# Performance work log

Measured on AMD Instinct MI355X. Metric: run time of the kernel, lower is better.

The kernel has to match this reference:

```python
import jax, jax.numpy as jnp
import numpy as np

B, N, C = 2, 2048, 768
H, HD = 12, 64
HID = 3072
LN_EPS = 1e-5
POL_EPS = 1e-6


def _layer_norm(x, g, b):
    m = jnp.mean(x, axis=-1, keepdims=True)
    v = jnp.mean(jnp.square(x - m), axis=-1, keepdims=True)
    return (x - m) * jax.lax.rsqrt(v + LN_EPS) * g + b


def _softmax_with_policy(attn, policy):
    # attn: [B,H,N,N], policy: [B,N,1]
    n = attn.shape[-1]
    ap = policy.reshape(policy.shape[0], 1, 1, n)  # [B,1,1,N]
    eye = jnp.eye(n, dtype=ap.dtype)[None, None]   # [1,1,N,N]
    ap = ap + (1.0 - ap) * eye                     # always attend to self
    attn = attn - jnp.max(attn, axis=-1, keepdims=True)
    attn = jnp.exp(attn.astype(jnp.float32)) * ap.astype(jnp.float32)
    attn = (attn + POL_EPS / n) / (jnp.sum(attn, axis=-1, keepdims=True) + POL_EPS)
    return attn


def setup_inputs() -> dict:
    key = jax.random.key(0)
    ks = jax.random.split(key, 12)
    s = lambda fan_in: 1.0 / np.sqrt(fan_in)
    x = jax.random.normal(ks[0], (B, N, C), dtype=jnp.float32)
    policy = (jax.random.uniform(ks[1], (B, N, 1)) > 0.5).astype(jnp.float32)
    return {
        "x": x,
        "policy": policy,
        "ln1_g": jnp.ones((C,), jnp.float32),
        "ln1_b": jnp.zeros((C,), jnp.float32),
        "qkv_w": jax.random.uniform(ks[2], (3 * H * HD, C), jnp.float32, -s(C), s(C)),
        "proj_w": jax.random.uniform(ks[3], (C, H * HD), jnp.float32, -s(H * HD), s(H * HD)),
        "proj_b": jnp.zeros((C,), jnp.float32),
        "ln2_g": jnp.ones((C,), jnp.float32),
        "ln2_b": jnp.zeros((C,), jnp.float32),
        "fc1_w": jax.random.uniform(ks[4], (HID, C), jnp.float32, -s(C), s(C)),
        "fc1_b": jnp.zeros((HID,), jnp.float32),
        "fc2_w": jax.random.uniform(ks[5], (C, HID), jnp.float32, -s(HID), s(HID)),
        "fc2_b": jnp.zeros((C,), jnp.float32),
    }


def reference(x, policy, ln1_g, ln1_b, qkv_w, proj_w, proj_b, ln2_g, ln2_b, fc1_w, fc1_b, fc2_w, fc2_b):
    b, n, c = x.shape
    scale = HD ** -0.5
    # --- attention branch (pre-LN) ---
    h = _layer_norm(x, ln1_g, ln1_b)
    qkv = (h @ qkv_w.T).reshape(b, n, 3, H, HD).transpose(2, 0, 3, 1, 4)  # [3,B,H,N,hd]
    q, k, v = qkv[0], qkv[1], qkv[2]
    attn = jnp.einsum("bhqd,bhkd->bhqk", q * scale, k)
    attn = _softmax_with_policy(attn, policy).astype(x.dtype)
    o = jnp.einsum("bhqk,bhkd->bhqd", attn, v).transpose(0, 2, 1, 3).reshape(b, n, H * HD)
    x = x + (o @ proj_w.T + proj_b)  # skip_lam = 1.0, dropout/drop_path = identity
    # --- MLP branch (pre-LN) ---
    h = _layer_norm(x, ln2_g, ln2_b)
    h = jax.nn.gelu(h @ fc1_w.T + fc1_b, approximate=False)  # torch nn.GELU = exact erf
    x = x + (h @ fc2_w.T + fc2_b)
    return x
```

## Files before the change

kernel.cpp:

```cpp
#include <hip/hip_runtime.h>

typedef unsigned short u16;
typedef unsigned int u32;
typedef float f32x4 __attribute__((ext_vector_type(4)));
typedef float f32x16 __attribute__((ext_vector_type(16)));
typedef __bf16 bf16x8 __attribute__((ext_vector_type(8)));
typedef u16 u16x4v __attribute__((ext_vector_type(4)));
typedef u32 u32x2 __attribute__((ext_vector_type(2)));
typedef u32 u32x4 __attribute__((ext_vector_type(4)));

#define NHEAD 12
#define NN 2048
#define CC 768

#define GLOBAL_AS __attribute__((address_space(1)))
#define LDS_AS __attribute__((address_space(3)))

__device__ __forceinline__ u16 tobf(float f) {
  __bf16 h = (__bf16)f;
  return __builtin_bit_cast(u16, h);
}
__device__ __forceinline__ float bf2f(u16 h) {
  u32 u = ((u32)h) << 16;
  return __builtin_bit_cast(float, u);
}
__device__ __forceinline__ u32 cvtpk(float lo, float hi) {
  u32 r;
  asm("v_cvt_pk_bf16_f32 %0, %1, %2" : "=v"(r) : "v"(lo), "v"(hi));
  return r;
}
__device__ __forceinline__ void plswap(u32& a, u32& b) {
  asm volatile("v_permlane32_swap_b32 %0, %1" : "+v"(a), "+v"(b));
}
__device__ __forceinline__ void plswapf(float& a, float& b) {
  asm volatile("v_permlane32_swap_b32 %0, %1" : "+v"(a), "+v"(b));
}

#define N4_QKV 442368
#define N4_PROJ 147456
#define N4_FC 589824
__global__ __launch_bounds__(256) void cvt4_kernel(
    const float* __restrict__ a, const float* __restrict__ b,
    const float* __restrict__ c, const float* __restrict__ d,
    u16* __restrict__ oa, u16* __restrict__ ob, u16* __restrict__ oc,
    u16* __restrict__ od) {
  int i = blockIdx.x * 256 + threadIdx.x;
  const float* src;
  u16* dst;
  if (i < N4_QKV) {
    src = a; dst = oa;
  } else if (i < N4_QKV + N4_PROJ) {
    i -= N4_QKV; src = b; dst = ob;
  } else if (i < N4_QKV + N4_PROJ + N4_FC) {
    i -= N4_QKV + N4_PROJ; src = c; dst = oc;
  } else {
    i -= N4_QKV + N4_PROJ + N4_FC; src = d; dst = od;
    if (i >= N4_FC) return;
  }
  float4 v = ((const float4*)src)[i];
  u16x4v o = {tobf(v.x), tobf(v.y), tobf(v.z), tobf(v.w)};
  ((u16x4v*)dst)[i] = o;
}

__global__ __launch_bounds__(256) void ln_kernel(const float* __restrict__ x,
                                                 const float* __restrict__ gw,
                                                 const float* __restrict__ bw,
                                                 u16* __restrict__ out) {
  int row = blockIdx.x * 4 + (threadIdx.x >> 6);
  int lane = threadIdx.x & 63;
  const float* xr = x + (size_t)row * CC + lane * 12;
  float v[12];
  *(float4*)&v[0] = *(const float4*)(xr + 0);
  *(float4*)&v[4] = *(const float4*)(xr + 4);
  *(float4*)&v[8] = *(const float4*)(xr + 8);
  float s = 0.f, sq = 0.f;
#pragma unroll
  for (int j = 0; j < 12; ++j) { s += v[j]; sq += v[j] * v[j]; }
#pragma unroll
  for (int o = 1; o < 64; o <<= 1) { s += __shfl_xor(s, o); sq += __shfl_xor(sq, o); }
  float mean = s * (1.f / CC);
  float var = sq * (1.f / CC) - mean * mean;
  float rs = rsqrtf(var + 1e-5f);
  u16 ob[12];
#pragma unroll
  for (int j = 0; j < 12; ++j) {
    int c = lane * 12 + j;
    ob[j] = tobf((v[j] - mean) * rs * gw[c] + bw[c]);
  }
  u32* orow = (u32*)(out + (size_t)row * CC + lane * 12);
#pragma unroll
  for (int j = 0; j < 6; ++j) orow[j] = (u32)ob[2 * j] | ((u32)ob[2 * j + 1] << 16);
}

template <int BM, int OB, int HASB, int ACT, int RES>
__global__ __launch_bounds__(256) void gemm_kernel(
    const u16* __restrict__ A, const u16* __restrict__ Bw,
    const float* __restrict__ bias, const float* __restrict__ res,
    void* __restrict__ Cout, int M, int N, int K) {
  constexpr int MW = BM / 2;
  constexpr int MF = MW / 16;
  __shared__ __align__(16) u16 Alds[BM * 64];
  __shared__ __align__(16) u16 Blds[128 * 64];
  const int tid = threadIdx.x;
  const int lane = tid & 63, wave = tid >> 6;
  const int l15 = lane & 15, g = lane >> 4;
  const int nx = gridDim.x;
  const int flat = blockIdx.y * nx + blockIdx.x;
  const int cpx = (nx * gridDim.y) >> 3;
  const int swz = (flat & 7) * cpx + (flat >> 3);
  const int bm = (swz % nx) * BM, bn = (swz / nx) * 128;
  const int wm = (wave >> 1) * MW, wn = (wave & 1) * 64;
  f32x4 acc[MF][4] = {};

  for (int kt = 0; kt < K; kt += 64) {
#pragma unroll
    for (int i = 0; i < BM / 32; ++i) {
      int ob_ = i * 4096 + wave * 1024;
      int lb = ob_ + lane * 16;
      int row = lb >> 7;
      int cb = (lb & 127) ^ ((row & 7) << 4);
      const u16* sa = A + (size_t)(bm + row) * K + kt + (cb >> 1);
      __builtin_amdgcn_global_load_lds((const GLOBAL_AS void*)sa,
                                       (LDS_AS void*)(Alds + (ob_ >> 1)), 16, 0, 0);
    }
#pragma unroll
    for (int i = 0; i < 4; ++i) {
      int ob_ = i * 4096 + wave * 1024;
      int lb = ob_ + lane * 16;
      int row = lb >> 7;
      int cb = (lb & 127) ^ ((row & 7) << 4);
      const u16* sb = Bw + (size_t)(bn + row) * K + kt + (cb >> 1);
      __builtin_amdgcn_global_load_lds((const GLOBAL_AS void*)sb,
                                       (LDS_AS void*)(Blds + (ob_ >> 1)), 16, 0, 0);
    }
    __syncthreads();
#pragma unroll
    for (int ks = 0; ks < 2; ++ks) {
      bf16x8 af[MF], bfr[4];
#pragma unroll
      for (int mi = 0; mi < MF; ++mi) {
        int row = wm + mi * 16 + l15;
        int cb = (ks * 64 + g * 16) ^ ((row & 7) << 4);
        af[mi] = *(const bf16x8*)&Alds[row * 64 + (cb >> 1)];
      }
#pragma unroll
      for (int ni = 0; ni < 4; ++ni) {
        int row = wn + ni * 16 + l15;
        int cb = (ks * 64 + g * 16) ^ ((row & 7) << 4);
        bfr[ni] = *(const bf16x8*)&Blds[row * 64 + (cb >> 1)];
      }
#pragma unroll
      for (int mi = 0; mi < MF; ++mi)
#pragma unroll
        for (int ni = 0; ni < 4; ++ni)
          acc[mi][ni] = __builtin_amdgcn_mfma_f32_16x16x32_bf16(af[mi], bfr[ni],
                                                                acc[mi][ni], 0, 0, 0);
    }
    __syncthreads();
  }
#pragma unroll
  for (int mi = 0; mi < MF; ++mi) {
#pragma unroll
    for (int ni = 0; ni < 4; ++ni) {
      int col = bn + wn + ni * 16 + l15;
      float bs = HASB ? bias[col] : 0.f;
#pragma unroll
      for (int r = 0; r < 4; ++r) {
        int rowm = bm + wm + mi * 16 + g * 4 + r;
        float v = acc[mi][ni][r] + bs;
        if (ACT) v = 0.5f * v * (1.f + erff(v * 0.70710678118654752f));
        if (RES) v += res[(size_t)rowm * N + col];
        if (OB)
          ((u16*)Cout)[(size_t)rowm * N + col] = tobf(v);
        else
          ((float*)Cout)[(size_t)rowm * N + col] = v;
      }
    }
  }
}

__global__ __launch_bounds__(256) void vsum_kernel(const u16* __restrict__ qkv,
                                                   float* __restrict__ vs) {
  int bh = blockIdx.x, q4 = blockIdx.y;
  int b = bh / NHEAD, h = bh % NHEAD;
  int d = threadIdx.x & 63, part = threadIdx.x >> 6;
  float s = 0.f;
  for (int n = q4 * 512 + part; n < q4 * 512 + 512; n += 4)
    s += bf2f(qkv[(size_t)(b * NN + n) * 2304 + 2 * CC + h * 64 + d]);
  __shared__ float red[256];
  red[threadIdx.x] = s;
  __syncthreads();
  if (threadIdx.x < 64) {
    float t = red[threadIdx.x] + red[threadIdx.x + 64] + red[threadIdx.x + 128] +
              red[threadIdx.x + 192];
    vs[q4 * (24 * 64) + bh * 64 + threadIdx.x] = t;
  }
}

__global__ __launch_bounds__(256) void scan_kernel(const float* __restrict__ policy,
                                                   int* __restrict__ ncbuf,
                                                   int* __restrict__ idxbuf) {
  int b = blockIdx.x, tid = threadIdx.x;
  float pv[8];
  *(float4*)&pv[0] = *(const float4*)&policy[b * NN + tid * 8];
  *(float4*)&pv[4] = *(const float4*)&policy[b * NN + tid * 8 + 4];
  int cnt = 0;
#pragma unroll
  for (int j = 0; j < 8; ++j) cnt += (pv[j] != 0.f) ? 1 : 0;
  __shared__ int sc[256];
  sc[tid] = cnt;
  __syncthreads();
  for (int off = 1; off < 256; off <<= 1) {
    int v = sc[tid];
    int add = (tid >= off) ? sc[tid - off] : 0;
    __syncthreads();
    sc[tid] = v + add;
    __syncthreads();
  }
  int base = sc[tid] - cnt;
#pragma unroll
  for (int j = 0; j < 8; ++j) {
    if (pv[j] != 0.f) idxbuf[b * NN + base++] = tid * 8 + j;
  }
  if (tid == 255) ncbuf[b] = sc[255];
}

__global__ __launch_bounds__(256) void gather_kernel(const u16* __restrict__ qkv,
                                                     const int* __restrict__ ncbuf,
                                                     const int* __restrict__ idxbuf,
                                                     u16* __restrict__ ckv) {
  int b = blockIdx.y;
  int nc = ncbuf[b];
  int ncp = (nc + 127) & ~127;
  int c = blockIdx.x * 256 + threadIdx.x;
  int j = c / 192, col = (c % 192) * 8;
  if (j >= ncp) return;
  uint4 val = {0, 0, 0, 0};
  if (j < nc) {
    int src = idxbuf[b * NN + j];
    val = *(const uint4*)&qkv[(size_t)(b * NN + src) * 2304 + CC + col];
  }
  *(uint4*)&ckv[(size_t)(b * NN + j) * 1536 + col] = val;
}

#define SCL2E 0.18033688f
#define TRRD(dst, addr, OFF) \
  asm volatile("ds_read_b64_tr_b16 %0, %1 offset:" OFF : "=v"(dst) : "v"(addr))

__global__ __launch_bounds__(256) void attn32_kernel(const u16* __restrict__ qkv,
                                                     const u16* __restrict__ ckv,
                                                     const int* __restrict__ ncbuf,
                                                     float* __restrict__ partO,
                                                     float* __restrict__ partlm) {
  __shared__ __align__(16) u16 Klds[2][4096];
  __shared__ __align__(16) u16 Vlds[2][4096];
  __shared__ float alf[4][32];
  const int bh = blockIdx.y, b = bh / NHEAD, h = bh % NHEAD;
  const int qt = blockIdx.x >> 1, half = blockIdx.x & 1;
  const int tid = threadIdx.x, lane = tid & 63, w = tid >> 6;
  const int l31 = lane & 31, hp = lane >> 5, b4 = (lane >> 4) & 1;
  const int q0 = qt * 128 + w * 32;
  const int nc = ncbuf[b];
  const int ncp = (nc + 127) & ~127;
  const int nh = ncp >> 1;
  const int nt = nh >> 6;
  const int kv0 = half * nh;
  const size_t adv = (size_t)64 * 1536;

  bf16x8 qf0, qf1, qf2, qf3;
  {
    const u16* qp = qkv + (size_t)(b * NN + q0 + l31) * 2304 + h * 64 + 8 * hp;
#pragma unroll
    for (int ds = 0; ds < 4; ++ds) {
      bf16x8 r = *(const bf16x8*)(qp + ds * 16);
      bf16x8 o;
#pragma unroll
      for (int j = 0; j < 8; ++j) o[j] = (__bf16)((float)r[j] * SCL2E);
      if (ds == 0) qf0 = o; else if (ds == 1) qf1 = o; else if (ds == 2) qf2 = o; else qf3 = o;
    }
  }

  const u16* ksrc[2];
  const u16* vsrcp[2];
#pragma unroll
  for (int c = 0; c < 2; ++c) {
    int lb = c * 4096 + w * 1024 + lane * 16;
    int row = lb >> 7;
    int cb = (lb & 127) ^ ((row & 7) << 4);
    ksrc[c] = ckv + (size_t)(b * NN + kv0 + row) * 1536 + h * 64 + (cb >> 1);
    int idx0 = (c * 256 + w * 64 + lane) * 8;
    int s0 = idx0 & 15, jj = (idx0 >> 4) & 3, b4v = (idx0 >> 6) & 1,
        pv = (idx0 >> 7) & 1, hv = (idx0 >> 8) & 1, dtv = (idx0 >> 9) & 1,
        mkv = (idx0 >> 10) & 3;
    int key = mkv * 16 + 8 * hv + 4 * pv + jj;
    int d0 = dtv * 32 + 16 * b4v + s0;
    vsrcp[c] = ckv + (size_t)(b * NN + kv0 + key) * 1536 + CC + h * 64 + d0;
  }
  auto stage = [&](int buf) {
#pragma unroll
    for (int c = 0; c < 2; ++c) {
      __builtin_amdgcn_global_load_lds((const GLOBAL_AS void*)ksrc[c],
                                       (LDS_AS void*)&Klds[buf][c * 2048 + w * 512], 16, 0, 0);
      __builtin_amdgcn_global_load_lds((const GLOBAL_AS void*)vsrcp[c],
                                       (LDS_AS void*)&Vlds[buf][c * 2048 + w * 512], 16, 0, 0);
      ksrc[c] += adv; vsrcp[c] += adv;
    }
  };

  stage(0);
  __syncthreads();

  float m_cur = -3.0e38f, m_true = -3.0e38f, l_run = 0.f;
  f32x16 accd[2] = {};
  const u32 vbase = (u32)(uintptr_t)(LDS_AS u16*)&Vlds[0][0] +
                    (u32)(2 * (lane & 15) + 128 * b4 + 512 * hp);

#pragma unroll 1
  for (int t = 0; t < nt; ++t) {
    const int cur = t & 1;
    if (t < nt - 1) stage(cur ^ 1);

    f32x16 sv0, sv1;
    {
      bf16x8 kf[4];
#pragma unroll
      for (int ds = 0; ds < 4; ++ds) {
        int row = l31;
        int cb = (32 * ds + 16 * hp) ^ ((row & 7) << 4);
        kf[ds] = *(const bf16x8*)((const char*)&Klds[cur][0] + row * 128 + cb);
      }
      f32x16 a = {};
      a = __builtin_amdgcn_mfma_f32_32x32x16_bf16(kf[0], qf0, a, 0, 0, 0);
      a = __builtin_amdgcn_mfma_f32_32x32x16_bf16(kf[1], qf1, a, 0, 0, 0);
      a = __builtin_amdgcn_mfma_f32_32x32x16_bf16(kf[2], qf2, a, 0, 0, 0);
      a = __builtin_amdgcn_mfma_f32_32x32x16_bf16(kf[3], qf3, a, 0, 0, 0);
      sv0 = a;
    }
    {
      bf16x8 kf[4];
#pragma unroll
      for (int ds = 0; ds < 4; ++ds) {
        int row = 32 + l31;
        int cb = (32 * ds + 16 * hp) ^ ((row & 7) << 4);
        kf[ds] = *(const bf16x8*)((const char*)&Klds[cur][0] + row * 128 + cb);
      }
      f32x16 a = {};
      a = __builtin_amdgcn_mfma_f32_32x32x16_bf16(kf[0], qf0, a, 0, 0, 0);
      a = __builtin_amdgcn_mfma_f32_32x32x16_bf16(kf[1], qf1, a, 0, 0, 0);
      a = __builtin_amdgcn_mfma_f32_32x32x16_bf16(kf[2], qf2, a, 0, 0, 0);
      a = __builtin_amdgcn_mfma_f32_32x32x16_bf16(kf[3], qf3, a, 0, 0, 0);
      sv1 = a;
    }

    u32x2 tr[4][2][2];
    {
      u32 vab = vbase + (u32)(cur * 8192);
      TRRD(tr[0][0][0], vab, "0");    TRRD(tr[0][0][1], vab, "256");
      TRRD(tr[0][1][0], vab, "1024"); TRRD(tr[0][1][1], vab, "1280");
      TRRD(tr[1][0][0], vab, "2048"); TRRD(tr[1][0][1], vab, "2304");
      TRRD(tr[1][1][0], vab, "3072"); TRRD(tr[1][1][1], vab, "3328");
      TRRD(tr[2][0][0], vab, "4096"); TRRD(tr[2][0][1], vab, "4352");
      TRRD(tr[3][0][0], vab, "6144"); TRRD(tr[3][0][1], vab, "6400");
      TRRD(tr[2][1][0], vab, "5120"); TRRD(tr[2][1][1], vab, "5376");
      TRRD(tr[3][1][0], vab, "7168"); TRRD(tr[3][1][1], vab, "7424");
    }

    float ta = fmaxf(fmaxf(sv0[0], sv0[1]), sv0[2]);
    float tb = fmaxf(fmaxf(sv0[3], sv0[4]), sv0[5]);
    float tc = fmaxf(fmaxf(sv0[6], sv0[7]), sv0[8]);
    float td = fmaxf(fmaxf(sv0[9], sv0[10]), sv0[11]);
    float te = fmaxf(fmaxf(sv0[12], sv0[13]), sv0[14]);
    float tf = fmaxf(fmaxf(sv0[15], sv1[0]), sv1[1]);
    float tg = fmaxf(fmaxf(sv1[2], sv1[3]), sv1[4]);
    float th = fmaxf(fmaxf(sv1[5], sv1[6]), sv1[7]);
    float ti = fmaxf(fmaxf(sv1[8], sv1[9]), sv1[10]);
    float tj = fmaxf(fmaxf(sv1[11], sv1[12]), sv1[13]);
    float tk = fmaxf(sv1[14], sv1[15]);
    float tmax = fmaxf(fmaxf(fmaxf(fmaxf(ta, tb), fmaxf(tc, td)),
                             fmaxf(fmaxf(te, tf), fmaxf(tg, th))),
                       fmaxf(fmaxf(ti, tj), tk));
    {
      float t1 = tmax, t2 = tmax;
      plswapf(t1, t2);
      tmax = fmaxf(t1, t2);
    }
    m_true = fmaxf(m_true, tmax);
    const bool defer = __all(tmax <= m_cur + 8.f);
    const float m_new = defer ? m_cur : fmaxf(m_cur, tmax);

    const int thr = nc - (kv0 + t * 64);
    float ev[32];
#pragma unroll
    for (int kt = 0; kt < 2; ++kt) {
#pragma unroll
      for (int i = 0; i < 4; ++i) {
#pragma unroll
        for (int rq = 0; rq < 4; ++rq) {
          int r = 4 * i + rq;
          int kidx = kt * 32 + 8 * i + 4 * hp + rq;
          float sval = kt ? sv1[r] : sv0[r];
          float e = __builtin_amdgcn_exp2f(sval - m_new);
          ev[kt * 16 + r] = (kidx < thr) ? e : 0.f;
        }
      }
    }
    u32 wv[16];
#pragma unroll
    for (int j = 0; j < 16; ++j) wv[j] = cvtpk(ev[2 * j], ev[2 * j + 1]);
    float ps[16];
#pragma unroll
    for (int j = 0; j < 16; ++j)
      ps[j] = __builtin_bit_cast(float, wv[j] << 16) +
              __builtin_bit_cast(float, wv[j] & 0xffff0000u);
#pragma unroll
    for (int s = 8; s > 0; s >>= 1)
#pragma unroll
      for (int j = 0; j < s; ++j) ps[j] += ps[j + s];
    float psum = ps[0];
    {
      float s1 = psum, s2 = psum;
      plswapf(s1, s2);
      psum = s1 + s2;
    }
    if (!defer) {
      float alpha = __builtin_amdgcn_exp2f(m_cur - m_new);
      l_run = l_run * alpha + psum;
      m_cur = m_new;
      if (lane < 32) alf[w][lane] = alpha;
      float4 aq0 = *(const float4*)&alf[w][4 * hp];
      float4 aq1 = *(const float4*)&alf[w][8 + 4 * hp];
      float4 aq2 = *(const float4*)&alf[w][16 + 4 * hp];
      float4 aq3 = *(const float4*)&alf[w][24 + 4 * hp];
#pragma unroll
      for (int dt = 0; dt < 2; ++dt) {
#pragma unroll
        for (int rq = 0; rq < 4; ++rq) {
          accd[dt][0 + rq] *= ((const float*)&aq0)[rq];
          accd[dt][4 + rq] *= ((const float*)&aq1)[rq];
          accd[dt][8 + rq] *= ((const float*)&aq2)[rq];
          accd[dt][12 + rq] *= ((const float*)&aq3)[rq];
        }
      }
    } else {
      l_run += psum;
    }

    u32 PK[4][4];
#pragma unroll
    for (int mk = 0; mk < 4; ++mk) {
      int bw_ = 8 * (mk >> 1) + 4 * (mk & 1);
      PK[mk][0] = wv[bw_ + 0];
      PK[mk][1] = wv[bw_ + 1];
      PK[mk][2] = wv[bw_ + 2];
      PK[mk][3] = wv[bw_ + 3];
      plswap(PK[mk][2], PK[mk][0]);
      plswap(PK[mk][3], PK[mk][1]);
    }

    asm volatile("s_waitcnt lgkmcnt(0)" ::: "memory");
    __builtin_amdgcn_sched_barrier(0);

#pragma unroll
    for (int mk = 0; mk < 4; ++mk) {
      u32x4 pk4 = {PK[mk][0], PK[mk][1], PK[mk][2], PK[mk][3]};
      bf16x8 pf = __builtin_bit_cast(bf16x8, pk4);
#pragma unroll
      for (int dt = 0; dt < 2; ++dt) {
        u32x4 vv = {tr[mk][dt][0].x, tr[mk][dt][0].y, tr[mk][dt][1].x, tr[mk][dt][1].y};
        bf16x8 vf = __builtin_bit_cast(bf16x8, vv);
        accd[dt] = __builtin_amdgcn_mfma_f32_32x32x16_bf16(pf, vf, accd[dt], 0, 0, 0);
      }
    }
    __syncthreads();
  }

  float sr = __builtin_amdgcn_exp2f(m_cur - m_true);
  if (lane < 32) {
    alf[w][lane] = sr;
    float2 lm = {l_run * sr, m_true};
    *(float2*)&partlm[2 * ((size_t)(half * 24 + bh) * 2048 + q0 + lane)] = lm;
  }
  float4 sq0 = *(const float4*)&alf[w][4 * hp];
  float4 sq1 = *(const float4*)&alf[w][8 + 4 * hp];
  float4 sq2 = *(const float4*)&alf[w][16 + 4 * hp];
  float4 sq3 = *(const float4*)&alf[w][24 + 4 * hp];
  float* pb2 = partO + ((size_t)(half * 24 + bh) * 2048) * 64;
#pragma unroll
  for (int dt = 0; dt < 2; ++dt) {
#pragma unroll
    for (int i = 0; i < 4; ++i) {
      float4 sqv = (i == 0) ? sq0 : (i == 1) ? sq1 : (i == 2) ? sq2 : sq3;
#pragma unroll
      for (int rq = 0; rq < 4; ++rq) {
        int row = q0 + 8 * i + 4 * hp + rq;
        pb2[(size_t)row * 64 + dt * 32 + l31] = accd[dt][4 * i + rq] * ((const float*)&sqv)[rq];
      }
    }
  }
}

__global__ __launch_bounds__(256) void merge_kernel(const float* __restrict__ partO,
                                                    const float* __restrict__ partlm,
                                                    const float* __restrict__ vs,
                                                    const float* __restrict__ policy,
                                                    const u16* __restrict__ qkv,
                                                    u16* __restrict__ o) {
  int rr = blockIdx.x * 4 + (threadIdx.x >> 6);
  int lane = threadIdx.x & 63;
  int bh = rr >> 11, q = rr & 2047;
  int b = bh / NHEAD, h = bh % NHEAD;
  const float* O1 = partO + ((size_t)bh * 2048 + q) * 64;
  const float* O2 = partO + ((size_t)(24 + bh) * 2048 + q) * 64;
  float2 lm1 = ((const float2*)partlm)[(size_t)bh * 2048 + q];
  float2 lm2 = ((const float2*)partlm)[(size_t)(24 + bh) * 2048 + q];
  float ms = fmaxf(lm1.y, lm2.y);
  float w1 = exp2f(lm1.y - ms), w2 = exp2f(lm2.y - ms);
  float num_d = 0.f, den_d = 0.f;
  if (policy[b * NN + q] == 0.f) {
    const u16* rowp = qkv + (size_t)(b * NN + q) * 2304 + h * 64 + lane;
    float qd = bf2f(rowp[0]);
    float kd = bf2f(rowp[CC]);
    float vv = bf2f(rowp[2 * CC]);
    float dp = qd * kd;
#pragma unroll
    for (int of = 1; of < 64; of <<= 1) dp += __shfl_xor(dp, of);
    float e = exp2f(dp * 0.18033688f - ms);
    num_d = e * vv;
    den_d = e;
  }
  float den = lm1.x * w1 + lm2.x * w2 + den_d + 1e-6f;
  float vsv = vs[bh * 64 + lane] + vs[1536 + bh * 64 + lane] +
              vs[3072 + bh * 64 + lane] + vs[4608 + bh * 64 + lane];
  float num = O1[lane] * w1 + O2[lane] * w2 + num_d + (1e-6f / 2048.f) * vsv;
  o[((size_t)(b * NN + q)) * CC + h * 64 + lane] = tobf(num / den);
}

extern "C" void kernel_launch(void* const* d_in, const int* in_sizes, int n_in,
                              void* d_out, int out_size, void* d_ws, size_t ws_size,
                              hipStream_t stream) {
  const float* x = (const float*)d_in[0];
  const float* policy = (const float*)d_in[1];
  const float* ln1g = (const float*)d_in[2];
  const float* ln1b = (const float*)d_in[3];
  const float* qkvw = (const float*)d_in[4];
  const float* projw = (const float*)d_in[5];
  const float* projb = (const float*)d_in[6];
  const float* ln2g = (const float*)d_in[7];
  const float* ln2b = (const float*)d_in[8];
  const float* fc1w = (const float*)d_in[9];
  const float* fc1b = (const float*)d_in[10];
  const float* fc2w = (const float*)d_in[11];
  const float* fc2b = (const float*)d_in[12];
  float* out = (float*)d_out;

  char* ws = (char*)d_ws;
  size_t off = 0;
  auto alloc = [&](size_t bytes) {
    void* p = ws + off;
    off = (off + bytes + 255) & ~(size_t)255;
    return p;
  };
  u16* wq = (u16*)alloc((size_t)2304 * 768 * 2);
  u16* wp = (u16*)alloc((size_t)768 * 768 * 2);
  u16* w1 = (u16*)alloc((size_t)3072 * 768 * 2);
  u16* w2 = (u16*)alloc((size_t)768 * 3072 * 2);
  u16* hbuf = (u16*)alloc((size_t)4096 * 768 * 2);
  u16* obuf = (u16*)alloc((size_t)4096 * 768 * 2);
  u16* qkv = (u16*)alloc((size_t)4096 * 2304 * 2);
  float* vs = (float*)alloc((size_t)4 * 24 * 64 * 4);
  int* ncbuf = (int*)alloc(2 * sizeof(int));
  int* idxbuf = (int*)alloc((size_t)2 * NN * sizeof(int));
  size_t unionOff = off;
  float* partO = (float*)alloc((size_t)2 * 24 * 2048 * 64 * 4);
  float* partlm = (float*)alloc((size_t)2 * 24 * 2048 * 2 * 4);
  float* x1 = (float*)(ws + unionOff);
  u16* ckv = hbuf;
  u16* f1 = obuf;

  cvt4_kernel<<<6912, 256, 0, stream>>>(qkvw, projw, fc1w, fc2w, wq, wp, w1, w2);

  ln_kernel<<<1024, 256, 0, stream>>>(x, ln1g, ln1b, hbuf);
  gemm_kernel<128, 1, 0, 0, 0><<<dim3(32, 18), 256, 0, stream>>>(
      hbuf, wq, nullptr, nullptr, qkv, 4096, 2304, 768);
  vsum_kernel<<<dim3(24, 4), 256, 0, stream>>>(qkv, vs);
  scan_kernel<<<2, 256, 0, stream>>>(policy, ncbuf, idxbuf);
  gather_kernel<<<dim3(1536, 2), 256, 0, stream>>>(qkv, ncbuf, idxbuf, ckv);
  attn32_kernel<<<dim3(32, 24), 256, 0, stream>>>(qkv, ckv, ncbuf, partO, partlm);
  merge_kernel<<<12288, 256, 0, stream>>>(partO, partlm, vs, policy, qkv, obuf);
  gemm_kernel<64, 0, 1, 0, 1><<<dim3(64, 6), 256, 0, stream>>>(
      obuf, wp, projb, x, x1, 4096, 768, 768);
  ln_kernel<<<1024, 256, 0, stream>>>(x1, ln2g, ln2b, hbuf);
  gemm_kernel<128, 1, 1, 1, 0><<<dim3(32, 24), 256, 0, stream>>>(
      hbuf, w1, fc1b, nullptr, f1, 4096, 3072, 768);
  gemm_kernel<64, 0, 1, 0, 1><<<dim3(64, 6), 256, 0, stream>>>(
      f1, w2, fc2b, x1, out, 4096, 768, 3072);
}
```

Before: 232.0 us.

## Double-buffer GEMM LDS tiles with async prefetch and use polynomial erf GELU

Splits the GEMM shared-memory tiles into two buffers. The next K-tile's global-to-LDS loads are issued before computing on the current tile, with explicit vmcnt waits and raw barriers replacing __syncthreads, so load latency overlaps MFMA work. The exact erff in the fused GELU epilogue is replaced by a rational polynomial approximation using hardware rcp and exp2. This doubles LDS use per block, which may lower occupancy, and introduces a small approximation error in GELU.

```diff
diff --git a/kernel.cpp b/kernel.cpp
--- a/kernel.cpp
+++ b/kernel.cpp
@@ -34,6 +34,19 @@
 }
 __device__ __forceinline__ void plswapf(float& a, float& b) {
   asm volatile("v_permlane32_swap_b32 %0, %1" : "+v"(a), "+v"(b));
+}
+__device__ __forceinline__ float gelu_erf(float v) {
+  float y = fabsf(v) * 0.70710678118654752f;
+  float t = __builtin_amdgcn_rcpf(fmaf(0.3275911f, y, 1.f));
+  float p = fmaf(1.061405429f, t, -1.453152027f);
+  p = fmaf(p, t, 1.421413741f);
+  p = fmaf(p, t, -0.284496736f);
+  p = fmaf(p, t, 0.254829592f);
+  p = p * t;
+  float e = __builtin_amdgcn_exp2f(-y * y * 1.44269504f);
+  float er = fmaf(-p, e, 1.f);
+  er = (v < 0.f) ? -er : er;
+  return 0.5f * v * (1.f + er);
 }
 
 #define N4_QKV 442368
@@ -99,8 +112,8 @@
     void* __restrict__ Cout, int M, int N, int K) {
   constexpr int MW = BM / 2;
   constexpr int MF = MW / 16;
-  __shared__ __align__(16) u16 Alds[BM * 64];
-  __shared__ __align__(16) u16 Blds[128 * 64];
+  __shared__ __align__(16) u16 Alds[2][BM * 64];
+  __shared__ __align__(16) u16 Blds[2][128 * 64];
   const int tid = threadIdx.x;
   const int lane = tid & 63, wave = tid >> 6;
   const int l15 = lane & 15, g = lane >> 4;
@@ -112,7 +125,7 @@
   const int wm = (wave >> 1) * MW, wn = (wave & 1) * 64;
   f32x4 acc[MF][4] = {};
 
-  for (int kt = 0; kt < K; kt += 64) {
+  auto stage = [&](int buf, int kt) {
 #pragma unroll
     for (int i = 0; i < BM / 32; ++i) {
       int ob_ = i * 4096 + wave * 1024;
@@ -121,7 +134,7 @@
       int cb = (lb & 127) ^ ((row & 7) << 4);
       const u16* sa = A + (size_t)(bm + row) * K + kt + (cb >> 1);
       __builtin_amdgcn_global_load_lds((const GLOBAL_AS void*)sa,
-                                       (LDS_AS void*)(Alds + (ob_ >> 1)), 16, 0, 0);
+                                       (LDS_AS void*)(&Alds[buf][0] + (ob_ >> 1)), 16, 0, 0);
     }
 #pragma unroll
     for (int i = 0; i < 4; ++i) {
@@ -131,9 +144,28 @@
       int cb = (lb & 127) ^ ((row & 7) << 4);
       const u16* sb = Bw + (size_t)(bn + row) * K + kt + (cb >> 1);
       __builtin_amdgcn_global_load_lds((const GLOBAL_AS void*)sb,
-                                       (LDS_AS void*)(Blds + (ob_ >> 1)), 16, 0, 0);
-    }
-    __syncthreads();
+                                       (LDS_AS void*)(&Blds[buf][0] + (ob_ >> 1)), 16, 0, 0);
+    }
+  };
+
+  const int nt = K >> 6;
+  stage(0, 0);
+#pragma unroll 1
+  for (int t = 0; t < nt; ++t) {
+    const int cur = t & 1;
+    if (t + 1 < nt) {
+      stage(cur ^ 1, (t + 1) * 64);
+      if constexpr (BM == 128) {
+        asm volatile("s_waitcnt vmcnt(8)" ::: "memory");
+      } else {
+        asm volatile("s_waitcnt vmcnt(6)" ::: "memory");
+      }
+    } else {
+      asm volatile("s_waitcnt vmcnt(0)" ::: "memory");
+    }
+    __builtin_amdgcn_sched_barrier(0);
+    __builtin_amdgcn_s_barrier();
+    __builtin_amdgcn_sched_barrier(0);
 #pragma unroll
     for (int ks = 0; ks < 2; ++ks) {
       bf16x8 af[MF], bfr[4];
@@ -141,13 +173,13 @@
       for (int mi = 0; mi < MF; ++mi) {
         int row = wm + mi * 16 + l15;
         int cb = (ks * 64 + g * 16) ^ ((row & 7) << 4);
-        af[mi] = *(const bf16x8*)&Alds[row * 64 + (cb >> 1)];
+        af[mi] = *(const bf16x8*)&Alds[cur][row * 64 + (cb >> 1)];
       }
 #pragma unroll
       for (int ni = 0; ni < 4; ++ni) {
         int row = wn + ni * 16 + l15;
         int cb = (ks * 64 + g * 16) ^ ((row & 7) << 4);
-        bfr[ni] = *(const bf16x8*)&Blds[row * 64 + (cb >> 1)];
+        bfr[ni] = *(const bf16x8*)&Blds[cur][row * 64 + (cb >> 1)];
       }
 #pragma unroll
       for (int mi = 0; mi < MF; ++mi)
@@ -156,7 +188,10 @@
           acc[mi][ni] = __builtin_amdgcn_mfma_f32_16x16x32_bf16(af[mi], bfr[ni],
                                                                 acc[mi][ni], 0, 0, 0);
     }
-    __syncthreads();
+    asm volatile("s_waitcnt lgkmcnt(0)" ::: "memory");
+    __builtin_amdgcn_sched_barrier(0);
+    __builtin_amdgcn_s_barrier();
+    __builtin_amdgcn_sched_barrier(0);
   }
 #pragma unroll
   for (int mi = 0; mi < MF; ++mi) {
@@ -168,7 +203,7 @@
       for (int r = 0; r < 4; ++r) {
         int rowm = bm + wm + mi * 16 + g * 4 + r;
         float v = acc[mi][ni][r] + bs;
-        if (ACT) v = 0.5f * v * (1.f + erff(v * 0.70710678118654752f));
+        if (ACT) v = gelu_erf(v);
         if (RES) v += res[(size_t)rowm * N + col];
         if (OB)
           ((u16*)Cout)[(size_t)rowm * N + col] = tobf(v);
```

Result: slower. 244.6 us (+5.5%).

## Stage GEMM epilogue through LDS for vectorized stores and use fast GELU

Applied to the files above, without the earlier changes.

The GEMM epilogue now writes accumulator results into swizzled shared memory, which reuses the staging buffers, and then has all threads issue coalesced 16-byte stores, with the residual add done in float4. The intent is to replace scattered 2- and 4-byte global stores and residual loads with wide, coalesced transactions. The exact erff in the GELU is also swapped for an Abramowitz-Stegun polynomial built on hardware rcp and exp2, which costs some accuracy (error around 1e-7 absolute). Shared memory use may grow for the fp32-output variants, and the extra barrier adds a sync.

```diff
diff --git a/kernel.cpp b/kernel.cpp
--- a/kernel.cpp
+++ b/kernel.cpp
@@ -34,6 +34,19 @@
 }
 __device__ __forceinline__ void plswapf(float& a, float& b) {
   asm volatile("v_permlane32_swap_b32 %0, %1" : "+v"(a), "+v"(b));
+}
+__device__ __forceinline__ float gelu_erf(float v) {
+  float y = fabsf(v) * 0.70710678118654752f;
+  float t = __builtin_amdgcn_rcpf(fmaf(0.3275911f, y, 1.f));
+  float p = fmaf(1.061405429f, t, -1.453152027f);
+  p = fmaf(p, t, 1.421413741f);
+  p = fmaf(p, t, -0.284496736f);
+  p = fmaf(p, t, 0.254829592f);
+  p = p * t;
+  float e = __builtin_amdgcn_exp2f(-y * y * 1.44269504f);
+  float er = fmaf(-p, e, 1.f);
+  er = (v < 0.f) ? -er : er;
+  return 0.5f * v * (1.f + er);
 }
 
 #define N4_QKV 442368
@@ -99,8 +112,12 @@
     void* __restrict__ Cout, int M, int N, int K) {
   constexpr int MW = BM / 2;
   constexpr int MF = MW / 16;
-  __shared__ __align__(16) u16 Alds[BM * 64];
-  __shared__ __align__(16) u16 Blds[128 * 64];
+  constexpr int STAGE_B = BM * 64 * 2 + 128 * 64 * 2;
+  constexpr int EPI_B = BM * 128 * (OB ? 2 : 4);
+  constexpr int SMEM_B = (STAGE_B > EPI_B) ? STAGE_B : EPI_B;
+  __shared__ __align__(16) u16 smem[SMEM_B / 2];
+  u16* Alds = smem;
+  u16* Blds = smem + BM * 64;
   const int tid = threadIdx.x;
   const int lane = tid & 63, wave = tid >> 6;
   const int l15 = lane & 15, g = lane >> 4;
@@ -158,23 +175,49 @@
     }
     __syncthreads();
   }
+
+  char* Clds = (char*)smem;
 #pragma unroll
   for (int mi = 0; mi < MF; ++mi) {
 #pragma unroll
     for (int ni = 0; ni < 4; ++ni) {
-      int col = bn + wn + ni * 16 + l15;
-      float bs = HASB ? bias[col] : 0.f;
+      int cl = wn + ni * 16 + l15;
+      float bs = HASB ? bias[bn + cl] : 0.f;
 #pragma unroll
       for (int r = 0; r < 4; ++r) {
-        int rowm = bm + wm + mi * 16 + g * 4 + r;
+        int rl = wm + mi * 16 + g * 4 + r;
         float v = acc[mi][ni][r] + bs;
-        if (ACT) v = 0.5f * v * (1.f + erff(v * 0.70710678118654752f));
-        if (RES) v += res[(size_t)rowm * N + col];
-        if (OB)
-          ((u16*)Cout)[(size_t)rowm * N + col] = tobf(v);
-        else
-          ((float*)Cout)[(size_t)rowm * N + col] = v;
-      }
+        if (ACT) v = gelu_erf(v);
+        if (OB) {
+          int byte_ = rl * 256 + ((cl * 2) ^ ((rl & 7) << 4));
+          *(u16*)(Clds + byte_) = tobf(v);
+        } else {
+          int byte_ = rl * 512 + ((cl * 4) ^ ((rl & 7) << 4));
+          *(float*)(Clds + byte_) = v;
+        }
+      }
+    }
+  }
+  __syncthreads();
+  constexpr int ROWB = OB ? 256 : 512;
+  constexpr int CPR = ROWB / 16;
+  constexpr int NITER = BM * CPR / 256;
+#pragma unroll
+  for (int i = 0; i < NITER; ++i) {
+    int c = i * 256 + tid;
+    int rl = c / CPR;
+    int cb = (c % CPR) * 16;
+    int sb = rl * ROWB + (cb ^ ((rl & 7) << 4));
+    uint4 val = *(const uint4*)(Clds + sb);
+    if (OB) {
+      *(uint4*)((u16*)Cout + (size_t)(bm + rl) * N + bn + (cb >> 1)) = val;
+    } else {
+      float4 v4 = __builtin_bit_cast(float4, val);
+      if (RES) {
+        float4 r4 = *(const float4*)(res + (size_t)(bm + rl) * N + bn + (cb >> 2));
+        v4.x += r4.x; v4.y += r4.y; v4.z += r4.z; v4.w += r4.w;
+      }
+      *(float4*)((float*)Cout + (size_t)(bm + rl) * N + bn + (cb >> 2)) = v4;
     }
   }
 }
```

Result: slower. 243.2 us (+4.9%).
